# Kernel optimization log

Measured on AMD Instinct MI355X. Metric: run time of the kernel, lower is better.

Reference implementation:

```python
import jax, jax.numpy as jnp
import numpy as np

B, N, C, H = 2, 2048, 1024, 16
D = C // H
EPS = 1e-5  # torch LayerNorm default


def layernorm(x, gamma, beta):
    mu = jnp.mean(x, axis=-1, keepdims=True)
    var = jnp.mean(jnp.square(x - mu), axis=-1, keepdims=True)
    return (x - mu) * jax.lax.rsqrt(var + EPS) * gamma + beta


def setup_inputs() -> dict:
    key = jax.random.key(0)
    ks = jax.random.split(key, 4)
    x = jax.random.normal(ks[0], (B, N, C), dtype=jnp.float32)
    w_qkv = jax.random.normal(ks[1], (3 * C, C), dtype=jnp.float32) * (C ** -0.5)
    w_proj = jax.random.normal(ks[2], (C, C), dtype=jnp.float32) * (C ** -0.5)
    return {
        "x": x,
        "w_qkv": w_qkv,
        "q_gamma": jnp.ones((C,), jnp.float32),
        "q_beta": jnp.zeros((C,), jnp.float32),
        "k_gamma": jnp.ones((C,), jnp.float32),
        "k_beta": jnp.zeros((C,), jnp.float32),
        "lpe_w": jnp.ones((C,), jnp.float32),
        "lpe_b": jnp.zeros((C,), jnp.float32),
        "w_proj": w_proj,
        "b_proj": jnp.zeros((C,), jnp.float32),
    }


def reference(x, w_qkv, q_gamma, q_beta, k_gamma, k_beta, lpe_w, lpe_b, w_proj, b_proj):
    b, n, c = x.shape
    scale = D ** -0.5
    qkv = jnp.einsum('bnc,fc->bnf', x, w_qkv)            # (B,N,3C)
    qkv = qkv.reshape(b, n, 3, H, D)
    q, k, v = qkv[:, :, 0], qkv[:, :, 1], qkv[:, :, 2]   # (B,N,H,D)
    # QK-norm: LayerNorm over flattened heads (dim C)
    q = layernorm(q.reshape(b, n, c), q_gamma, q_beta).reshape(b, n, H, D)
    k = layernorm(k.reshape(b, n, c), k_gamma, k_beta).reshape(b, n, H, D)
    # LPE: depthwise 1x1x1 conv == per-channel affine on v
    v_lpe = v.reshape(b, n, c) * lpe_w + lpe_b           # (B,N,C)
    # attention
    attn = jnp.einsum('bqhd,bkhd->bhqk', q * scale, k)   # (B,H,N,N)
    attn = jax.nn.softmax(attn, axis=-1)
    out = jnp.einsum('bhqk,bkhd->bqhd', attn, v).reshape(b, n, c)
    y = jnp.einsum('bnc,oc->bno', out + v_lpe, w_proj) + b_proj
    return y
```

## Files before the change

kernel.cpp:

```cpp
#include <hip/hip_runtime.h>
#include <stdint.h>

#define Bdim 2
#define Ndim 2048
#define Cdim 1024
#define Hdim 16
#define Ddim 64
#define Fdim 3072
#define Mdim 4096

typedef unsigned int  u32;
typedef unsigned short u16;
typedef float f32x4 __attribute__((ext_vector_type(4)));
typedef short s16x8 __attribute__((ext_vector_type(8)));
typedef unsigned short u16x4 __attribute__((ext_vector_type(4)));
typedef unsigned int u32x2 __attribute__((ext_vector_type(2)));
typedef unsigned int u32x4 __attribute__((ext_vector_type(4)));

__device__ __forceinline__ u16 f2b(float f) {
  u32 u = __builtin_bit_cast(u32, f);
  u += 0x7FFFu + ((u >> 16) & 1u);
  return (u16)(u >> 16);
}
__device__ __forceinline__ float b2f(u16 h) {
  return __builtin_bit_cast(float, (u32)h << 16);
}
__device__ __forceinline__ u32 cvtpk(float a, float b) {
  u32 d;
  asm("v_cvt_pk_bf16_f32 %0, %1, %2" : "=v"(d) : "v"(a), "v"(b));
  return d;
}
__device__ __forceinline__ float rexp2(float x) { return __builtin_amdgcn_exp2f(x); }
__device__ __forceinline__ f32x4 mfma16(s16x8 a, s16x8 b, f32x4 c) {
  return __builtin_amdgcn_mfma_f32_16x16x32_bf16(a, b, c, 0, 0, 0);
}
__device__ __forceinline__ void gl_lds16(const void* g, void* l) {
  __builtin_amdgcn_global_load_lds(
      (const __attribute__((address_space(1))) void*)g,
      (__attribute__((address_space(3))) void*)l, 16, 0, 0);
}
__device__ __forceinline__ bool is_bf16(const void* qg) {
  return *(const u32*)qg == 0x3F803F80u;
}

__global__ __launch_bounds__(256)
void k_prep(const void* x, const void* wq, const void* wp,
            const void* g0, const void* g1, const void* g2, const void* g3,
            const void* g4, const void* g5, const void* g6,
            u16* xb, u16* wqb, u16* wpb, float* prm) {
  const int i = blockIdx.x * 256 + threadIdx.x;
  const bool isbf = is_bf16(g0);
  const void* src; u16* dst; int k;
  if (i < 524288)       { src = x;  dst = xb;  k = i; }
  else if (i < 917504)  { src = wq; dst = wqb; k = i - 524288; }
  else if (i < 1048576) { src = wp; dst = wpb; k = i - 917504; }
  else {
    const int j = i - 1048576;
    if (j >= 1792) return;
    const int fi = j * 4;
    const int pi = fi >> 10, off = fi & 1023;
    const void* s = (pi == 0) ? g0 : (pi == 1) ? g1 : (pi == 2) ? g2
                  : (pi == 3) ? g3 : (pi == 4) ? g4 : (pi == 5) ? g5 : g6;
    float4 v;
    if (isbf) {
      u16x4 h = *(const u16x4*)((const u16*)s + off);
      v.x = b2f(h.x); v.y = b2f(h.y); v.z = b2f(h.z); v.w = b2f(h.w);
    } else {
      v = *(const float4*)((const float*)s + off);
    }
    *(float4*)(prm + fi) = v;
    return;
  }
  if (isbf) {
    ((u32x4*)dst)[k] = ((const u32x4*)src)[k];
  } else {
    const float4 a = ((const float4*)src)[2 * k];
    const float4 b = ((const float4*)src)[2 * k + 1];
    u32x4 o;
    o.x = cvtpk(a.x, a.y);
    o.y = cvtpk(a.z, a.w);
    o.z = cvtpk(b.x, b.y);
    o.w = cvtpk(b.z, b.w);
    ((u32x4*)dst)[k] = o;
  }
}

__global__ __launch_bounds__(256)
void k_gemm_qkv(const u16* __restrict__ A, const u16* __restrict__ W,
                u16* __restrict__ Cb, u16* __restrict__ vTp,
                int Msz, int Nsz, int Ksz) {
  __shared__ __align__(16) char lds[32768];
  const int tid = threadIdx.x;
  const int lane = tid & 63;
  const int wm = (tid >> 6) >> 1, wn = (tid >> 6) & 1;
  const int g = lane >> 4, cl = lane & 15;
  const int nwg = gridDim.x * gridDim.y;
  const int lid = blockIdx.y * gridDim.x + blockIdx.x;
  const int cpx = nwg >> 3;
  const int swz = (lid & 7) * cpx + (lid >> 3);
  const int row0 = (swz / gridDim.x) * 128, col0 = (swz % gridDim.x) * 128;
  const int KT = Ksz >> 5;

  f32x4 acc[4][4] = {};

  auto stage = [&](int buf, int kt) {
    const int k0 = kt << 5;
#pragma unroll
    for (int iss = 0; iss < 2; ++iss) {
      const int t = iss * 256 + tid;
      const int r = t >> 2;
      const int ss = (t & 3) ^ ((r >> 1) & 3);
      gl_lds16(A + (size_t)(row0 + r) * Ksz + k0 + ss * 8, &lds[buf * 16384 + t * 16]);
      gl_lds16(W + (size_t)(col0 + r) * Ksz + k0 + ss * 8, &lds[buf * 16384 + 8192 + t * 16]);
    }
  };

  stage(0, 0);
  __syncthreads();
  int cur = 0;
  for (int kt = 0; kt < KT; ++kt) {
    if (kt + 1 < KT) stage(cur ^ 1, kt + 1);
    const char* Ab = &lds[cur * 16384];
    const char* Bb = &lds[cur * 16384 + 8192];
    s16x8 af[4], bfr[4];
#pragma unroll
    for (int mi = 0; mi < 4; ++mi) {
      const int r = wm * 64 + mi * 16 + cl;
      const int s = g ^ ((r >> 1) & 3);
      af[mi] = *(const s16x8*)(Ab + r * 64 + s * 16);
    }
#pragma unroll
    for (int nj = 0; nj < 4; ++nj) {
      const int r = wn * 64 + nj * 16 + cl;
      const int s = g ^ ((r >> 1) & 3);
      bfr[nj] = *(const s16x8*)(Bb + r * 64 + s * 16);
    }
#pragma unroll
    for (int mi = 0; mi < 4; ++mi)
#pragma unroll
      for (int nj = 0; nj < 4; ++nj)
        acc[mi][nj] = mfma16(af[mi], bfr[nj], acc[mi][nj]);
    __syncthreads();
    cur ^= 1;
  }

#pragma unroll
  for (int mi = 0; mi < 4; ++mi)
#pragma unroll
    for (int nj = 0; nj < 4; ++nj) {
      const int m0 = row0 + wm * 64 + mi * 16 + g * 4;
      const int nbase = col0 + wn * 64 + nj * 16;
      const int n = nbase + cl;
      if (nbase >= 2048) {
        const int h = (nbase - 2048) >> 6;
        const int d = ((nbase - 2048) & 63) + cl;
        u16x4 pk;
#pragma unroll
        for (int r = 0; r < 4; ++r) pk[r] = f2b(acc[mi][nj][r]);
        *(u16x4*)(vTp + (size_t)h * (64 * 4096) + (size_t)d * 4096 + m0) = pk;
      } else {
#pragma unroll
        for (int r = 0; r < 4; ++r)
          Cb[(size_t)(m0 + r) * Nsz + n] = f2b(acc[mi][nj][r]);
      }
    }
}

__global__ __launch_bounds__(256)
void k_gemm_n64(const u16* __restrict__ A, const u16* __restrict__ W,
                void* __restrict__ Cout, const float* __restrict__ bias,
                const void* __restrict__ qg) {
  __shared__ __align__(16) char lds[24576];
  const int tid = threadIdx.x;
  const int lane = tid & 63;
  const int w = tid >> 6;
  const int g = lane >> 4, cl = lane & 15;
  const int nwg = gridDim.x * gridDim.y;
  const int lid = blockIdx.y * gridDim.x + blockIdx.x;
  const int cpx = nwg >> 3;
  const int swz = (lid & 7) * cpx + (lid >> 3);
  const int row0 = (swz / gridDim.x) * 128, col0 = (swz % gridDim.x) * 64;
  const int KT = Cdim >> 5;

  f32x4 acc[2][4] = {};

  auto stage = [&](int buf, int kt) {
    const int k0 = kt << 5;
#pragma unroll
    for (int iss = 0; iss < 2; ++iss) {
      const int t = iss * 256 + tid;
      const int r = t >> 2;
      const int ss = (t & 3) ^ ((r >> 1) & 3);
      gl_lds16(A + (size_t)(row0 + r) * Cdim + k0 + ss * 8, &lds[buf * 12288 + t * 16]);
    }
    {
      const int r = tid >> 2;
      const int ss = (tid & 3) ^ ((r >> 1) & 3);
      gl_lds16(W + (size_t)(col0 + r) * Cdim + k0 + ss * 8, &lds[buf * 12288 + 8192 + tid * 16]);
    }
  };

  stage(0, 0);
  __syncthreads();
  int cur = 0;
  for (int kt = 0; kt < KT; ++kt) {
    if (kt + 1 < KT) stage(cur ^ 1, kt + 1);
    const char* Ab = &lds[cur * 12288];
    const char* Bb = &lds[cur * 12288 + 8192];
    s16x8 af[2], bfr[4];
#pragma unroll
    for (int mi = 0; mi < 2; ++mi) {
      const int r = w * 32 + mi * 16 + cl;
      const int s = g ^ ((r >> 1) & 3);
      af[mi] = *(const s16x8*)(Ab + r * 64 + s * 16);
    }
#pragma unroll
    for (int nj = 0; nj < 4; ++nj) {
      const int r = nj * 16 + cl;
      const int s = g ^ ((r >> 1) & 3);
      bfr[nj] = *(const s16x8*)(Bb + r * 64 + s * 16);
    }
#pragma unroll
    for (int mi = 0; mi < 2; ++mi)
#pragma unroll
      for (int nj = 0; nj < 4; ++nj)
        acc[mi][nj] = mfma16(af[mi], bfr[nj], acc[mi][nj]);
    __syncthreads();
    cur ^= 1;
  }

  const u32 oflag = is_bf16(qg) ? 1u : 0u;
#pragma unroll
  for (int mi = 0; mi < 2; ++mi)
#pragma unroll
    for (int nj = 0; nj < 4; ++nj) {
      const int m0 = row0 + w * 32 + mi * 16 + g * 4;
      const int n = col0 + nj * 16 + cl;
#pragma unroll
      for (int r = 0; r < 4; ++r) {
        float v = acc[mi][nj][r] + bias[n];
        if (oflag) ((u16*)Cout)[(size_t)(m0 + r) * Cdim + n] = f2b(v);
        else       ((float*)Cout)[(size_t)(m0 + r) * Cdim + n] = v;
      }
    }
}

__global__ __launch_bounds__(256)
void k_ln(u16* __restrict__ qkv, const float* __restrict__ prm) {
  const int tid = threadIdx.x, lane = tid & 63, w = tid >> 6;
  const int m = blockIdx.x * 2 + (w >> 1);
  const int seg = w & 1;
  u16* s = qkv + (size_t)m * Fdim + seg * 1024 + lane * 16;

  u16x4 v[4];
#pragma unroll
  for (int j = 0; j < 4; ++j) v[j] = *(const u16x4*)(s + j * 4);
  float x[16];
#pragma unroll
  for (int j = 0; j < 4; ++j)
#pragma unroll
    for (int r = 0; r < 4; ++r) x[j * 4 + r] = b2f(v[j][r]);

  float sum = 0.f, ssq = 0.f;
#pragma unroll
  for (int k = 0; k < 16; ++k) { sum += x[k]; ssq += x[k] * x[k]; }
#pragma unroll
  for (int off = 32; off >= 1; off >>= 1) {
    sum += __shfl_xor(sum, off);
    ssq += __shfl_xor(ssq, off);
  }
  const float mu = sum * (1.0f / 1024.0f);
  const float var = ssq * (1.0f / 1024.0f) - mu * mu;
  const float rstd = rsqrtf(var + 1e-5f);
  const float scl = (seg == 0) ? (0.125f * 1.4426950408889634f) : 1.0f;

  const float* gam = prm + seg * 2048 + lane * 16;
  const float* bet = gam + 1024;
  float4 g4[4], b4[4];
#pragma unroll
  for (int j = 0; j < 4; ++j) {
    g4[j] = *(const float4*)(gam + j * 4);
    b4[j] = *(const float4*)(bet + j * 4);
  }
  u32x4 o0, o1;
#pragma unroll
  for (int p = 0; p < 8; ++p) {
    const int k0 = 2 * p, k1 = 2 * p + 1;
    const float y0 = ((x[k0] - mu) * rstd * (&g4[k0 >> 2].x)[k0 & 3] + (&b4[k0 >> 2].x)[k0 & 3]) * scl;
    const float y1 = ((x[k1] - mu) * rstd * (&g4[k1 >> 2].x)[k1 & 3] + (&b4[k1 >> 2].x)[k1 & 3]) * scl;
    const u32 wd = cvtpk(y0, y1);
    if (p < 4) o0[p] = wd; else o1[p - 4] = wd;
  }
  *(u32x4*)(s) = o0;
  *(u32x4*)(s + 8) = o1;
}

__global__ __launch_bounds__(256, 2)
void k_attn(const u16* __restrict__ qkv, const u16* __restrict__ vT,
            u16* __restrict__ pin, const float* __restrict__ prm) {
  const int bid = blockIdx.x;
  const int qt = (bid >> 3) & 15;
  const int bh = (bid & 7) * 4 + (bid >> 7);
  const int b = bh >> 4, h = bh & 15;
  const int tid = threadIdx.x, lane = tid & 63, w = tid >> 6;
  const int g = lane >> 4, cl = lane & 15;
  const int c7 = cl & 7;
  const int mrow0 = b * Ndim + qt * 128;
  const int NT = Ndim / 64;

  const u16* Qg  = qkv + (size_t)mrow0 * Fdim + h * 64;
  const u16* Kg  = qkv + (size_t)(b * Ndim) * Fdim + Cdim + h * 64;
  const u16* vTg = vT + (size_t)h * (64 * 4096) + b * Ndim;

  __shared__ __align__(16) char klds[4][8192];
  __shared__ __align__(16) char vlds[4][8192];
  __shared__ __align__(16) char plds[4][4096];

  s16x8 bq[2][2];
#pragma unroll
  for (int qb = 0; qb < 2; ++qb)
#pragma unroll
    for (int kc = 0; kc < 2; ++kc)
      bq[qb][kc] = *(const s16x8*)(Qg + (size_t)(w * 32 + qb * 16 + cl) * Fdim + kc * 32 + g * 8);

  f32x4 o[2][4] = {};
  float mr[2] = {-1e30f, -1e30f};
  float lr[2] = {0.f, 0.f};

  const char* akp0 = &klds[0][cl * 128 + (((0 + g) ^ c7) << 4)];
  const char* akp1 = &klds[0][cl * 128 + (((4 + g) ^ c7) << 4)];
  const char* avp0 = &vlds[0][cl * 128 + (((0 + g) ^ c7) << 4)];
  const char* avp1 = &vlds[0][cl * 128 + (((4 + g) ^ c7) << 4)];
  char* pwp[4];
#pragma unroll
  for (int nj = 0; nj < 4; ++nj)
    pwp[nj] = &plds[w][cl * 128 + ((nj * 32 + g * 8) ^ (c7 << 4))];
  const char* bpp0 = &plds[w][cl * 128 + ((0  + g * 16) ^ (c7 << 4))];
  const char* bpp1 = &plds[w][cl * 128 + ((64 + g * 16) ^ (c7 << 4))];

  const int r0 = tid >> 3;
  const int ss0 = ((tid & 7) ^ (r0 & 7)) * 8;
  const u16* kp = Kg + (size_t)r0 * Fdim + ss0;
  const u16* vp = vTg + (size_t)r0 * 4096 + ss0;
  char* kd = &klds[0][tid * 16];
  char* vd = &vlds[0][tid * 16];

#pragma unroll
  for (int pt = 0; pt < 2; ++pt) {
    gl_lds16(kp, kd + pt * 8192);
    gl_lds16(kp + (size_t)32 * Fdim, kd + pt * 8192 + 4096);
    gl_lds16(vp, vd + pt * 8192);
    gl_lds16(vp + (size_t)32 * 4096, vd + pt * 8192 + 4096);
    kp += (size_t)64 * Fdim;
    vp += 64;
  }

#define ATTN_BODY(BUF, PRE, WAITINSN)                                         \
  {                                                                           \
    asm volatile(WAITINSN ::: "memory");                                      \
    __builtin_amdgcn_s_barrier();                                             \
    __builtin_amdgcn_sched_barrier(0);                                        \
    if (PRE) {                                                                \
      char* kdd = kd + ((((BUF) + 2) & 3) * 8192);                            \
      char* vdd = vd + ((((BUF) + 2) & 3) * 8192);                            \
      gl_lds16(kp, kdd);                                                      \
      gl_lds16(kp + (size_t)32 * Fdim, kdd + 4096);                           \
      gl_lds16(vp, vdd);                                                      \
      gl_lds16(vp + (size_t)32 * 4096, vdd + 4096);                           \
      kp += (size_t)64 * Fdim;                                                \
      vp += 64;                                                               \
    }                                                                         \
    s16x8 ak[4][2];                                                           \
    _Pragma("unroll") for (int nj = 0; nj < 4; ++nj) {                        \
      ak[nj][0] = *(const s16x8*)(akp0 + (BUF) * 8192 + nj * 2048);           \
      ak[nj][1] = *(const s16x8*)(akp1 + (BUF) * 8192 + nj * 2048);           \
    }                                                                         \
                       \
    f32x4 sv[2][4];                                                           \
    __builtin_amdgcn_s_setprio(1);                                            \
    _Pragma("unroll") for (int qb = 0; qb < 2; ++qb)                          \
      _Pragma("unroll") for (int nj = 0; nj < 4; ++nj) {                      \
        f32x4 z = {0.f, 0.f, 0.f, 0.f};                                       \
        z = mfma16(ak[nj][0], bq[qb][0], z);                                  \
        z = mfma16(ak[nj][1], bq[qb][1], z);                                  \
        sv[qb][nj] = z;                                                       \
      }                                                                       \
    __builtin_amdgcn_s_setprio(0);                                            \
    _Pragma("unroll") for (int qb = 0; qb < 2; ++qb) {                        \
      float a0 = fmaxf(fmaxf(sv[qb][0][0], sv[qb][0][1]), sv[qb][0][2]);      \
      float a1 = fmaxf(fmaxf(sv[qb][0][3], sv[qb][1][0]), sv[qb][1][1]);      \
      float a2 = fmaxf(fmaxf(sv[qb][1][2], sv[qb][1][3]), sv[qb][2][0]);      \
      float a3 = fmaxf(fmaxf(sv[qb][2][1], sv[qb][2][2]), sv[qb][2][3]);      \
      float a4 = fmaxf(fmaxf(sv[qb][3][0], sv[qb][3][1]), sv[qb][3][2]);      \
      float b0v = fmaxf(fmaxf(a0, a1), a2);                                   \
      float b1v = fmaxf(fmaxf(a3, a4), sv[qb][3][3]);                         \
      float mx = fmaxf(b0v, b1v);                                             \
      if (!__all(mx <= mr[qb] + 7.0f)) {                                      \
        mx = fmaxf(mx, __shfl_xor(mx, 16));                                   \
        mx = fmaxf(mx, __shfl_xor(mx, 32));                                   \
        const float mn = fmaxf(mr[qb], mx);                                   \
        const float corr = rexp2(mr[qb] - mn);                                \
        mr[qb] = mn;                                                          \
        lr[qb] *= corr;                                                       \
        o[qb][0] *= corr; o[qb][1] *= corr;                                   \
        o[qb][2] *= corr; o[qb][3] *= corr;                                   \
      }                                                                       \
      const float mrq = mr[qb];                                               \
      float ssum = 0.f;                                                       \
      _Pragma("unroll") for (int nj = 0; nj < 4; ++nj) {                      \
        const float p0 = rexp2(sv[qb][nj][0] - mrq);                          \
        const float p1 = rexp2(sv[qb][nj][1] - mrq);                          \
        const float p2 = rexp2(sv[qb][nj][2] - mrq);                          \
        const float p3 = rexp2(sv[qb][nj][3] - mrq);                          \
        ssum += (p0 + p1) + (p2 + p3);                                        \
        u32x2 pk2;                                                            \
        pk2.x = cvtpk(p0, p1);                                                \
        pk2.y = cvtpk(p2, p3);                                                \
        *(u32x2*)(pwp[nj] + qb * 2048) = pk2;                                 \
      }                                                                       \
      lr[qb] += ssum;                                                         \
    }                                                                         \
                  \
    asm volatile("s_waitcnt lgkmcnt(0)" ::: "memory");                        \
    __builtin_amdgcn_sched_barrier(0);                                        \
    s16x8 av[4][2];                                                           \
    _Pragma("unroll") for (int dc = 0; dc < 4; ++dc) {                        \
      av[dc][0] = *(const s16x8*)(avp0 + (BUF) * 8192 + dc * 2048);           \
      av[dc][1] = *(const s16x8*)(avp1 + (BUF) * 8192 + dc * 2048);           \
    }                                                                         \
    _Pragma("unroll") for (int qb = 0; qb < 2; ++qb) {                        \
      const s16x8 bp0 = *(const s16x8*)(bpp0 + qb * 2048);                    \
      const s16x8 bp1 = *(const s16x8*)(bpp1 + qb * 2048);                    \
      __builtin_amdgcn_s_setprio(1);                                          \
      _Pragma("unroll") for (int dc = 0; dc < 4; ++dc) {                      \
        o[qb][dc] = mfma16(av[dc][0], bp0, o[qb][dc]);                        \
        o[qb][dc] = mfma16(av[dc][1], bp1, o[qb][dc]);                        \
      }                                                                       \
      __builtin_amdgcn_s_setprio(0);                                          \
    }                                                                         \
  }

  for (int t = 0; t + 4 < NT; t += 4) {
    ATTN_BODY(0, true, "s_waitcnt vmcnt(4)");
    ATTN_BODY(1, true, "s_waitcnt vmcnt(4)");
    ATTN_BODY(2, true, "s_waitcnt vmcnt(4)");
    ATTN_BODY(3, true, "s_waitcnt vmcnt(4)");
  }
  ATTN_BODY(0, true,  "s_waitcnt vmcnt(4)");
  ATTN_BODY(1, true,  "s_waitcnt vmcnt(4)");
  ATTN_BODY(2, false, "s_waitcnt vmcnt(4)");
  ATTN_BODY(3, false, "s_waitcnt vmcnt(0)");
#undef ATTN_BODY

#pragma unroll
  for (int qb = 0; qb < 2; ++qb) {
    const int q = w * 32 + qb * 16 + cl;
    const int m = mrow0 + q;
    const int nseq = qt * 128 + q;
    float lt = lr[qb];
    lt += __shfl_xor(lt, 16);
    lt += __shfl_xor(lt, 32);
    const float inv = 1.0f / lt;
#pragma unroll
    for (int dc = 0; dc < 4; ++dc) {
      const int d0 = dc * 16 + g * 4;
      const int c = h * 64 + d0;
      const float4 lw = *(const float4*)(prm + 4096 + c);
      const float4 lb = *(const float4*)(prm + 5120 + c);
      float vr[4];
#pragma unroll
      for (int r = 0; r < 4; ++r) {
        const float vv = b2f(vTg[(size_t)(d0 + r) * 4096 + nseq]);
        vr[r] = o[qb][dc][r] * inv + vv * (&lw.x)[r] + (&lb.x)[r];
      }
      u32x2 ov;
      ov.x = cvtpk(vr[0], vr[1]);
      ov.y = cvtpk(vr[2], vr[3]);
      *(u32x2*)(pin + (size_t)m * Cdim + c) = ov;
    }
  }
}

extern "C" void kernel_launch(void* const* d_in, const int* in_sizes, int n_in,
                              void* d_out, int out_size, void* d_ws, size_t ws_size,
                              hipStream_t stream) {
  (void)in_sizes; (void)n_in; (void)out_size; (void)ws_size;
  char* ws = (char*)d_ws;
  float* prm    = (float*)(ws + 256);
  u16*   xb     = (u16*)(ws + 32768);
  u16*   wqkvb  = (u16*)(ws + 32768 + 8388608);
  u16*   wprojb = (u16*)(ws + 32768 + 8388608 + 6291456);
  u16*   qkv    = (u16*)(ws + 32768 + 8388608 + 6291456 + 2097152);
  u16*   vT     = (u16*)(ws + 32768 + 8388608 + 6291456 + 2097152 + 25165824);
  u16*   pin    = xb;

  k_prep<<<4103, 256, 0, stream>>>(d_in[0], d_in[1], d_in[8],
                                   d_in[2], d_in[3], d_in[4], d_in[5],
                                   d_in[6], d_in[7], d_in[9],
                                   xb, wqkvb, wprojb, prm);

  k_gemm_qkv<<<dim3(Fdim / 128, Mdim / 128), 256, 0, stream>>>(
      xb, wqkvb, qkv, vT, Mdim, Fdim, Cdim);

  k_ln<<<Mdim / 2, 256, 0, stream>>>(qkv, prm);

  k_attn<<<dim3(512), 256, 0, stream>>>(qkv, vT, pin, prm);

  k_gemm_n64<<<dim3(Cdim / 64, Mdim / 128), 256, 0, stream>>>(
      pin, wprojb, d_out, prm + 6144, d_in[2]);
}
```

Measured before the change: 127.1 us.

## Deepen GEMM load pipelines to multi-stage rings with explicit vmcnt waits

Both the QKV GEMM and the N64 projection GEMM move from double-buffered LDS staging with two syncs per step to a 3- or 4-deep LDS ring. Each ring prefetches two k-tiles ahead, guarded by explicit s_waitcnt vmcnt counts and a single barrier per step. The loops are fully unrolled with fixed trip counts, and MFMA sections get raised wave priority via s_setprio. The aim is to hide global-to-LDS latency and cut barrier stalls, at the cost of more LDS per block, which may reduce occupancy. It also hardcodes K=1024.

New measurement: 125.6 us. No clear change (-1.2%).

```diff
diff --git a/kernel.cpp b/kernel.cpp
--- a/kernel.cpp
+++ b/kernel.cpp
@@ -89,7 +89,7 @@
 void k_gemm_qkv(const u16* __restrict__ A, const u16* __restrict__ W,
                 u16* __restrict__ Cb, u16* __restrict__ vTp,
                 int Msz, int Nsz, int Ksz) {
-  __shared__ __align__(16) char lds[32768];
+  __shared__ __align__(16) char lds[49152];
   const int tid = threadIdx.x;
   const int lane = tid & 63;
   const int wm = (tid >> 6) >> 1, wn = (tid >> 6) & 1;
@@ -99,7 +99,6 @@
   const int cpx = nwg >> 3;
   const int swz = (lid & 7) * cpx + (lid >> 3);
   const int row0 = (swz / gridDim.x) * 128, col0 = (swz % gridDim.x) * 128;
-  const int KT = Ksz >> 5;
 
   f32x4 acc[4][4] = {};
 
@@ -115,34 +114,44 @@
     }
   };
 
+#define G1_BODY(BUF, T, PRE, WAITINSN)                                        \
+  {                                                                           \
+    asm volatile(WAITINSN ::: "memory");                                      \
+    __builtin_amdgcn_s_barrier();                                             \
+    __builtin_amdgcn_sched_barrier(0);                                        \
+    if (PRE) stage(((BUF) + 2) % 3, (T) + 2);                                 \
+    const char* Ab = &lds[(BUF) * 16384];                                     \
+    const char* Bb = &lds[(BUF) * 16384 + 8192];                              \
+    s16x8 af[4], bfr[4];                                                      \
+    _Pragma("unroll") for (int mi = 0; mi < 4; ++mi) {                        \
+      const int r = wm * 64 + mi * 16 + cl;                                   \
+      const int s = g ^ ((r >> 1) & 3);                                       \
+      af[mi] = *(const s16x8*)(Ab + r * 64 + s * 16);                         \
+    }                                                                         \
+    _Pragma("unroll") for (int nj = 0; nj < 4; ++nj) {                        \
+      const int r = wn * 64 + nj * 16 + cl;                                   \
+      const int s = g ^ ((r >> 1) & 3);                                       \
+      bfr[nj] = *(const s16x8*)(Bb + r * 64 + s * 16);                        \
+    }                                                                         \
+    __builtin_amdgcn_s_setprio(1);                                            \
+    _Pragma("unroll") for (int mi = 0; mi < 4; ++mi)                          \
+      _Pragma("unroll") for (int nj = 0; nj < 4; ++nj)                        \
+        acc[mi][nj] = mfma16(af[mi], bfr[nj], acc[mi][nj]);                   \
+    __builtin_amdgcn_s_setprio(0);                                            \
+  }
+
   stage(0, 0);
-  __syncthreads();
-  int cur = 0;
-  for (int kt = 0; kt < KT; ++kt) {
-    if (kt + 1 < KT) stage(cur ^ 1, kt + 1);
-    const char* Ab = &lds[cur * 16384];
-    const char* Bb = &lds[cur * 16384 + 8192];
-    s16x8 af[4], bfr[4];
-#pragma unroll
-    for (int mi = 0; mi < 4; ++mi) {
-      const int r = wm * 64 + mi * 16 + cl;
-      const int s = g ^ ((r >> 1) & 3);
-      af[mi] = *(const s16x8*)(Ab + r * 64 + s * 16);
-    }
-#pragma unroll
-    for (int nj = 0; nj < 4; ++nj) {
-      const int r = wn * 64 + nj * 16 + cl;
-      const int s = g ^ ((r >> 1) & 3);
-      bfr[nj] = *(const s16x8*)(Bb + r * 64 + s * 16);
-    }
-#pragma unroll
-    for (int mi = 0; mi < 4; ++mi)
-#pragma unroll
-      for (int nj = 0; nj < 4; ++nj)
-        acc[mi][nj] = mfma16(af[mi], bfr[nj], acc[mi][nj]);
-    __syncthreads();
-    cur ^= 1;
-  }
+  stage(1, 1);
+  int t = 0;
+  for (int c = 0; c < 10; ++c) {
+    G1_BODY(0, t + 0, true, "s_waitcnt vmcnt(4)");
+    G1_BODY(1, t + 1, true, "s_waitcnt vmcnt(4)");
+    G1_BODY(2, t + 2, true, "s_waitcnt vmcnt(4)");
+    t += 3;
+  }
+  G1_BODY(0, 30, false, "s_waitcnt vmcnt(4)");
+  G1_BODY(1, 31, false, "s_waitcnt vmcnt(0)");
+#undef G1_BODY
 
 #pragma unroll
   for (int mi = 0; mi < 4; ++mi)
@@ -170,7 +179,7 @@
 void k_gemm_n64(const u16* __restrict__ A, const u16* __restrict__ W,
                 void* __restrict__ Cout, const float* __restrict__ bias,
                 const void* __restrict__ qg) {
-  __shared__ __align__(16) char lds[24576];
+  __shared__ __align__(16) char lds[49152];
   const int tid = threadIdx.x;
   const int lane = tid & 63;
   const int w = tid >> 6;
@@ -180,7 +189,6 @@
   const int cpx = nwg >> 3;
   const int swz = (lid & 7) * cpx + (lid >> 3);
   const int row0 = (swz / gridDim.x) * 128, col0 = (swz % gridDim.x) * 64;
-  const int KT = Cdim >> 5;
 
   f32x4 acc[2][4] = {};
 
@@ -193,41 +201,52 @@
       const int ss = (t & 3) ^ ((r >> 1) & 3);
       gl_lds16(A + (size_t)(row0 + r) * Cdim + k0 + ss * 8, &lds[buf * 12288 + t * 16]);
     }
-    {
-      const int r = tid >> 2;
-      const int ss = (tid & 3) ^ ((r >> 1) & 3);
-      gl_lds16(W + (size_t)(col0 + r) * Cdim + k0 + ss * 8, &lds[buf * 12288 + 8192 + tid * 16]);
-    }
+    const int r = tid >> 2;
+    const int ss = (tid & 3) ^ ((r >> 1) & 3);
+    gl_lds16(W + (size_t)(col0 + r) * Cdim + k0 + ss * 8, &lds[buf * 12288 + 8192 + tid * 16]);
   };
 
+#define G2_BODY(BUF, T, PRE, WAITINSN)                                        \
+  {                                                                           \
+    asm volatile(WAITINSN ::: "memory");                                      \
+    __builtin_amdgcn_s_barrier();                                             \
+    __builtin_amdgcn_sched_barrier(0);                                        \
+    if (PRE) stage(((BUF) + 2) & 3, (T) + 2);                                 \
+    const char* Ab = &lds[(BUF) * 12288];                                     \
+    const char* Bb = &lds[(BUF) * 12288 + 8192];                              \
+    s16x8 af[2], bfr[4];                                                      \
+    _Pragma("unroll") for (int mi = 0; mi < 2; ++mi) {                        \
+      const int r = w * 32 + mi * 16 + cl;                                    \
+      const int s = g ^ ((r >> 1) & 3);                                       \
+      af[mi] = *(const s16x8*)(Ab + r * 64 + s * 16);                         \
+    }                                                                         \
+    _Pragma("unroll") for (int nj = 0; nj < 4; ++nj) {                        \
+      const int r = nj * 16 + cl;                                             \
+      const int s = g ^ ((r >> 1) & 3);                                       \
+      bfr[nj] = *(const s16x8*)(Bb + r * 64 + s * 16);                        \
+    }                                                                         \
+    __builtin_amdgcn_s_setprio(1);                                            \
+    _Pragma("unroll") for (int mi = 0; mi < 2; ++mi)                          \
+      _Pragma("unroll") for (int nj = 0; nj < 4; ++nj)                        \
+        acc[mi][nj] = mfma16(af[mi], bfr[nj], acc[mi][nj]);                   \
+    __builtin_amdgcn_s_setprio(0);                                            \
+  }
+
   stage(0, 0);
-  __syncthreads();
-  int cur = 0;
-  for (int kt = 0; kt < KT; ++kt) {
-    if (kt + 1 < KT) stage(cur ^ 1, kt + 1);
-    const char* Ab = &lds[cur * 12288];
-    const char* Bb = &lds[cur * 12288 + 8192];
-    s16x8 af[2], bfr[4];
-#pragma unroll
-    for (int mi = 0; mi < 2; ++mi) {
-      const int r = w * 32 + mi * 16 + cl;
-      const int s = g ^ ((r >> 1) & 3);
-      af[mi] = *(const s16x8*)(Ab + r * 64 + s * 16);
-    }
-#pragma unroll
-    for (int nj = 0; nj < 4; ++nj) {
-      const int r = nj * 16 + cl;
-      const int s = g ^ ((r >> 1) & 3);
-      bfr[nj] = *(const s16x8*)(Bb + r * 64 + s * 16);
-    }
-#pragma unroll
-    for (int mi = 0; mi < 2; ++mi)
-#pragma unroll
-      for (int nj = 0; nj < 4; ++nj)
-        acc[mi][nj] = mfma16(af[mi], bfr[nj], acc[mi][nj]);
-    __syncthreads();
-    cur ^= 1;
-  }
+  stage(1, 1);
+  int t = 0;
+  for (int c = 0; c < 7; ++c) {
+    G2_BODY(0, t + 0, true, "s_waitcnt vmcnt(3)");
+    G2_BODY(1, t + 1, true, "s_waitcnt vmcnt(3)");
+    G2_BODY(2, t + 2, true, "s_waitcnt vmcnt(3)");
+    G2_BODY(3, t + 3, true, "s_waitcnt vmcnt(3)");
+    t += 4;
+  }
+  G2_BODY(0, 28, true,  "s_waitcnt vmcnt(3)");
+  G2_BODY(1, 29, true,  "s_waitcnt vmcnt(3)");
+  G2_BODY(2, 30, false, "s_waitcnt vmcnt(3)");
+  G2_BODY(3, 31, false, "s_waitcnt vmcnt(0)");
+#undef G2_BODY
 
   const u32 oflag = is_bf16(qg) ? 1u : 0u;
 #pragma unroll
```
